# Kernel optimization log

Hardware: AMD Instinct MI355X
Metric: run time of the kernel (lower is better)

## Reference

```python
import jax, jax.numpy as jnp
import numpy as np

NU, NM, E, L, B = 20000, 10000, 64, 3, 8192
SLOPE = 0.01  # torch leaky_relu default negative_slope


def _xavier(key, shape):
    fan_in, fan_out = shape[-1], shape[-2] if len(shape) >= 2 else shape[-1]
    limit = np.sqrt(6.0 / (fan_in + fan_out)).astype(np.float32)
    return jax.random.uniform(key, shape, jnp.float32, -limit, limit)


def setup_inputs() -> dict:
    key = jax.random.key(0)
    ks = jax.random.split(key, 12)
    user_adj = jax.random.uniform(ks[0], (NU, NM), jnp.float32)
    movie_adj = jax.random.uniform(ks[1], (NM, NU), jnp.float32)
    user_id = jax.random.randint(ks[2], (B,), 0, NU)
    movie_id = jax.random.randint(ks[3], (B,), 0, NM)
    user_emb = _xavier(ks[4], (NU, E))
    movie_emb = _xavier(ks[5], (NM, E))
    user_Ws = _xavier(ks[6], (L, E, E))
    user_bs = jnp.zeros((L, E), jnp.float32)
    movie_Ws = _xavier(ks[7], (L, E, E))
    movie_bs = jnp.zeros((L, E), jnp.float32)
    out_W = _xavier(ks[8], ((L + 1) * E, 1))
    out_b = jnp.zeros((1,), jnp.float32)
    return {
        "user_adj": user_adj, "movie_adj": movie_adj,
        "user_id": user_id, "movie_id": movie_id,
        "user_emb": user_emb, "movie_emb": movie_emb,
        "user_Ws": user_Ws, "user_bs": user_bs,
        "movie_Ws": movie_Ws, "movie_bs": movie_bs,
        "out_W": out_W, "out_b": out_b,
    }


def reference(user_adj, movie_adj, user_id, movie_id,
              user_emb, movie_emb, user_Ws, user_bs,
              movie_Ws, movie_bs, out_W, out_b):
    # dropout=0, carry_alpha=0, use_agate=False -> layer-0 embeddings are the tables
    us = [user_emb]   # list of [NU, E]
    ms = [movie_emb]  # list of [NM, E]
    n_layers = user_Ws.shape[0]
    for l in range(n_layers):
        # layer(adj @ other) + layer(self) == (adj @ other + self) @ W.T + 2*b
        u_new = jax.nn.leaky_relu(
            (user_adj @ ms[-1] + us[-1]) @ user_Ws[l].T + 2.0 * user_bs[l], SLOPE)
        m_new = jax.nn.leaky_relu(
            (movie_adj @ us[-1] + ms[-1]) @ movie_Ws[l].T + 2.0 * movie_bs[l], SLOPE)
        us.append(u_new)
        ms.append(m_new)
    # gather per-interaction embeddings at every depth, multiply, concat -> [B,(L+1)*E]
    inter = jnp.concatenate([u[user_id] * m[movie_id] for u, m in zip(us, ms)], axis=1)
    scores = (inter @ out_W + out_b).reshape(-1)  # [B]
    return scores, us[-1], ms[-1]
```

## Files before the change

### kernel.cpp

```cpp
#include <hip/hip_runtime.h>
#include <hip/hip_bf16.h>

typedef __attribute__((ext_vector_type(4))) float f32x4;
typedef __attribute__((ext_vector_type(8))) short short8;
typedef __attribute__((ext_vector_type(8))) __bf16 bf16x8;
typedef __attribute__((ext_vector_type(8))) unsigned char u8x8;

union FragU { bf16x8 h; short8 s; };
union F8 { f32x4 v[2]; float f[8]; };

typedef const __attribute__((address_space(1))) void gvoid_t;
typedef __attribute__((address_space(3))) void lvoid_t;

static __device__ __forceinline__ void gload16(const void* g, void* l) {
  __builtin_amdgcn_global_load_lds((gvoid_t*)g, (lvoid_t*)l, 16, 0, 0);
}

static __device__ __forceinline__ short8 cvt8(const f32x4 a0, const f32x4 a1) {
  bf16x8 hv;
  hv[0] = (__bf16)a0[0]; hv[1] = (__bf16)a0[1];
  hv[2] = (__bf16)a0[2]; hv[3] = (__bf16)a0[3];
  hv[4] = (__bf16)a1[0]; hv[5] = (__bf16)a1[1];
  hv[6] = (__bf16)a1[2]; hv[7] = (__bf16)a1[3];
  FragU u; u.h = hv; return u.s;
}

static __device__ __forceinline__ unsigned long long pack8_u8(
    const f32x4 a0, const f32x4 a1) {
  F8 u; u.v[0] = a0; u.v[1] = a1;
  unsigned long long r = 0;
  #pragma unroll
  for (int j = 0; j < 8; ++j) {
    unsigned int q = (unsigned int)(u.f[j] * 255.f + 0.5f);
    r |= (unsigned long long)(q & 255u) << (8 * j);
  }
  return r;
}

__global__ __launch_bounds__(256) void gemm_l0(
    const float* __restrict__ Au, const __bf16* __restrict__ BTu,
    unsigned char* __restrict__ AcU, float* __restrict__ Pu,
    int Mu, int Ku, int KTu, int padKu,
    const float* __restrict__ Am, const __bf16* __restrict__ BTm,
    unsigned char* __restrict__ AcM, float* __restrict__ Pm,
    int Mm, int Km, int KTm, int padKm,
    int nbU, int rbU, int rbM)
{
  __shared__ float  sA[2][4096];
  __shared__ __bf16 sB[2][2048];

  const int t = threadIdx.x;
  const int w = t >> 6;
  const int lane = t & 63;
  const int r = lane & 15;
  const int g = lane >> 4;

  const float* A; const __bf16* BT; unsigned char* Ac; float* P;
  int M, K, KT, Kpad, rowBlk, split;
  {
    int bx = blockIdx.x;
    if (bx < nbU) {
      A = Au; BT = BTu; Ac = AcU; P = Pu; M = Mu; K = Ku; KT = KTu; Kpad = padKu;
      rowBlk = bx % rbU; split = bx / rbU;
    } else {
      int b2 = bx - nbU;
      A = Am; BT = BTm; Ac = AcM; P = Pm; M = Mm; K = Km; KT = KTm; Kpad = padKm;
      rowBlk = b2 % rbM; split = b2 / rbM;
    }
  }
  const int rowBase = rowBlk * 128;
  const int NS = Kpad >> 5;
  const int s0 = split * 64;
  const int ns = min(64, NS - s0);

  f32x4 acc[2][4];
  #pragma unroll
  for (int m = 0; m < 2; ++m)
    #pragma unroll
    for (int n = 0; n < 4; ++n)
      acc[m][n] = (f32x4){0.f, 0.f, 0.f, 0.f};

  const float* aRowP[4];
  int aOff[4];
  #pragma unroll
  for (int i = 0; i < 4; ++i) {
    int idx = i * 256 + t;
    int rr = idx >> 3;
    int p  = idx & 7;
    int rowg = rowBase + rr; if (rowg > M - 1) rowg = M - 1;
    aRowP[i] = A + (size_t)rowg * K;
    aOff[i] = (p ^ (rr & 7)) << 2;
  }
  const __bf16* bSrc = BT + (size_t)(w * 16 + (lane >> 2)) * Kpad
                     + (size_t)(((lane & 3) ^ ((lane >> 3) & 3)) * 8);

  auto stage = [&](int buf, int h) {
    const int kk = (s0 + h) * 32;
    #pragma unroll
    for (int i = 0; i < 4; ++i) {
      int ke = kk + aOff[i];
      if (ke > K - 4) ke = K - 4;
      gload16(aRowP[i] + ke, &sA[buf][i * 1024 + w * 256]);
    }
    gload16(bSrc + kk, &sB[buf][w * 512]);
  };

  auto cons = [&](int buf, int h) {
    const int k32 = s0 + h;
    const bool ok = (k32 * 32 + g * 8) < K;
    const short8 z8 = {0, 0, 0, 0, 0, 0, 0, 0};
    FragU aF[2], bF[4];
    unsigned long long a8[2];
    #pragma unroll
    for (int m = 0; m < 2; ++m) {
      const float* rowp = &sA[buf][(w * 32 + m * 16 + r) * 32];
      f32x4 a0 = *(const f32x4*)(rowp + (((2 * g)     ^ (r & 7)) << 2));
      f32x4 a1 = *(const f32x4*)(rowp + (((2 * g + 1) ^ (r & 7)) << 2));
      aF[m].s = ok ? cvt8(a0, a1) : z8;
      a8[m] = ok ? pack8_u8(a0, a1) : 0ull;
    }
    const int gb = g ^ ((r >> 1) & 3);
    #pragma unroll
    for (int n = 0; n < 4; ++n)
      bF[n].s = *(const short8*)&sB[buf][(n * 16 + r) * 32 + gb * 8];
    #pragma unroll
    for (int m = 0; m < 2; ++m)
      #pragma unroll
      for (int n = 0; n < 4; ++n)
        acc[m][n] = __builtin_amdgcn_mfma_f32_16x16x32_bf16(
            aF[m].s, bF[n].s, acc[m][n], 0, 0, 0);
    const int kt = k32 >> 1, ks = k32 & 1;
    unsigned char* cp = Ac + ((size_t)rowBlk * KT + kt) * 8192
                      + (size_t)ks * 4096 + (size_t)lane * 8;
    *(unsigned long long*)(cp + (w * 2 + 0) * 512) = a8[0];
    *(unsigned long long*)(cp + (w * 2 + 1) * 512) = a8[1];
  };

  stage(0, 0);

  for (int h = 0; h < ns; ++h) {
    asm volatile("s_waitcnt vmcnt(0)" ::: "memory");
    __builtin_amdgcn_s_barrier();
    asm volatile("" ::: "memory");
    if (h + 1 < ns) stage((h + 1) & 1, h + 1);
    cons(h & 1, h);
  }

  float* Pp = P + (size_t)split * M * 64;
  #pragma unroll
  for (int m = 0; m < 2; ++m) {
    #pragma unroll
    for (int j = 0; j < 4; ++j) {
      const int row = rowBase + w * 32 + m * 16 + g * 4 + j;
      if (row < M) {
        #pragma unroll
        for (int n = 0; n < 4; ++n)
          Pp[(size_t)row * 64 + n * 16 + r] = acc[m][n][j];
      }
    }
  }
}

__global__ __launch_bounds__(256) void gemm_l12(
    const unsigned char* __restrict__ AcU, const __bf16* __restrict__ BTu,
    float* __restrict__ Pu, int Mu, int KTu, int padKu,
    const unsigned char* __restrict__ AcM, const __bf16* __restrict__ BTm,
    float* __restrict__ Pm, int Mm, int KTm, int padKm,
    int nbU, int rbU, int rbM, int SPS)
{
  __shared__ unsigned char sA[2][8192];
  __shared__ __bf16 sB[2][4096];

  const int t = threadIdx.x;
  const int w = t >> 6;
  const int lane = t & 63;
  const int r = lane & 15;
  const int g = lane >> 4;

  const unsigned char* Ac; const __bf16* BT; float* P;
  int M, KT, Kpad, rowBlk, split;
  {
    int bx = blockIdx.x;
    if (bx < nbU) {
      Ac = AcU; BT = BTu; P = Pu; M = Mu; KT = KTu; Kpad = padKu;
      rowBlk = bx % rbU; split = bx / rbU;
    } else {
      int b2 = bx - nbU;
      Ac = AcM; BT = BTm; P = Pm; M = Mm; KT = KTm; Kpad = padKm;
      rowBlk = b2 % rbM; split = b2 / rbM;
    }
  }
  const int rowBase = rowBlk * 128;
  const int s0 = split * SPS;
  const int ns = min(SPS, KT - s0);

  f32x4 acc[2][4];
  #pragma unroll
  for (int m = 0; m < 2; ++m)
    #pragma unroll
    for (int n = 0; n < 4; ++n)
      acc[m][n] = (f32x4){0.f, 0.f, 0.f, 0.f};

  const unsigned char* aB = Ac + (size_t)rowBlk * KT * 8192
                          + (size_t)w * 1024 + (size_t)lane * 16;
  const int browl = w * 16 + (lane >> 2);
  const int bgr = (lane & 3) ^ ((browl >> 1) & 3);
  const __bf16* bB = BT + (size_t)browl * Kpad + (size_t)bgr * 8;

  auto stage = [&](int buf, int hh) {
    const size_t tb = (size_t)(s0 + hh) * 8192;
    gload16(aB + tb,        &sA[buf][w * 1024]);
    gload16(aB + tb + 4096, &sA[buf][4096 + w * 1024]);
    const int k0 = (s0 + hh) * 64;
    gload16(bB + k0,      &sB[buf][w * 512]);
    gload16(bB + k0 + 32, &sB[buf][2048 + w * 512]);
  };

  auto cons = [&](int buf) {
    FragU aF[2][2], bF[2][4];
    #pragma unroll
    for (int ks = 0; ks < 2; ++ks) {
      #pragma unroll
      for (int m = 0; m < 2; ++m) {
        u8x8 by = *(const u8x8*)&sA[buf][ks * 4096 + (w * 2 + m) * 512 + lane * 8];
        bf16x8 hv;
        #pragma unroll
        for (int j = 0; j < 8; ++j) hv[j] = (__bf16)(float)by[j];
        aF[ks][m].h = hv;
      }
      #pragma unroll
      for (int n = 0; n < 4; ++n) {
        const int rowl = n * 16 + r;
        const int gg = g ^ ((rowl >> 1) & 3);
        bF[ks][n].s = *(const short8*)&sB[buf][ks * 2048 + rowl * 32 + gg * 8];
      }
    }
    #pragma unroll
    for (int ks = 0; ks < 2; ++ks)
      #pragma unroll
      for (int m = 0; m < 2; ++m)
        #pragma unroll
        for (int n = 0; n < 4; ++n)
          acc[m][n] = __builtin_amdgcn_mfma_f32_16x16x32_bf16(
              aF[ks][m].s, bF[ks][n].s, acc[m][n], 0, 0, 0);
  };

  stage(0, 0);

  for (int h = 0; h < ns; ++h) {
    asm volatile("s_waitcnt vmcnt(0)" ::: "memory");
    __builtin_amdgcn_s_barrier();
    asm volatile("" ::: "memory");
    if (h + 1 < ns) stage((h + 1) & 1, h + 1);
    cons(h & 1);
  }

  const float inv = 1.f / 255.f;
  float* Pp = P + (size_t)split * M * 64;
  #pragma unroll
  for (int m = 0; m < 2; ++m) {
    #pragma unroll
    for (int j = 0; j < 4; ++j) {
      const int row = rowBase + w * 32 + m * 16 + g * 4 + j;
      if (row < M) {
        #pragma unroll
        for (int n = 0; n < 4; ++n)
          Pp[(size_t)row * 64 + n * 16 + r] = acc[m][n][j] * inv;
      }
    }
  }
}

__global__ __launch_bounds__(256) void transpose_cvt(
    const float* __restrict__ in, __bf16* __restrict__ out, int K, int Kpad)
{
  __shared__ float tile[64][65];
  const int t = threadIdx.x;
  const int k0 = blockIdx.x * 64;
  #pragma unroll
  for (int i = 0; i < 4; ++i) {
    int f = t + i * 256;
    int k = f >> 4;
    int cc = (f & 15) << 2;
    if (k0 + k < K) {
      f32x4 v = *(const f32x4*)(in + (size_t)(k0 + k) * 64 + cc);
      tile[k][cc + 0] = v[0]; tile[k][cc + 1] = v[1];
      tile[k][cc + 2] = v[2]; tile[k][cc + 3] = v[3];
    }
  }
  __syncthreads();
  const int c = t >> 2;
  const int kc = (t & 3) << 4;
  #pragma unroll
  for (int h = 0; h < 2; ++h) {
    int kk = kc + h * 8;
    FragU p;
    if (k0 + kk < K) {
      #pragma unroll
      for (int j = 0; j < 8; ++j) p.h[j] = (__bf16)tile[kk + j][c];
    } else {
      p.s = (short8){0,0,0,0,0,0,0,0};
    }
    *(short8*)(out + (size_t)c * Kpad + k0 + kk) = p.s;
  }
}

__global__ __launch_bounds__(256) void layer_reduce(
    const float* __restrict__ P, int S,
    const float* __restrict__ self, const float* __restrict__ W,
    const float* __restrict__ b, float* __restrict__ out, int M)
{
  __shared__ float xs[4][64];
  const int t = threadIdx.x;
  const int c = t & 63;
  const int grp = t >> 6;
  const int row = blockIdx.x * 4 + grp;
  if (row < M) {
    float x = self[(size_t)row * 64 + c];
    for (int s = 0; s < S; ++s)
      x += P[(size_t)s * M * 64 + (size_t)row * 64 + c];
    xs[grp][c] = x;
  }
  __syncthreads();
  if (row >= M) return;
  float acc = 0.f;
  const f32x4* Wc = (const f32x4*)(W + c * 64);
  #pragma unroll
  for (int k4 = 0; k4 < 16; ++k4) {
    f32x4 wv = Wc[k4];
    acc += xs[grp][k4 * 4 + 0] * wv[0] + xs[grp][k4 * 4 + 1] * wv[1]
         + xs[grp][k4 * 4 + 2] * wv[2] + xs[grp][k4 * 4 + 3] * wv[3];
  }
  float v = acc + 2.0f * b[c];
  out[(size_t)row * 64 + c] = (v > 0.f) ? v : 0.01f * v;
}

__global__ __launch_bounds__(256) void gather_score(
    const int* __restrict__ uid, const int* __restrict__ mid,
    const float* __restrict__ u0, const float* __restrict__ u1,
    const float* __restrict__ u2, const float* __restrict__ u3,
    const float* __restrict__ m0, const float* __restrict__ m1,
    const float* __restrict__ m2, const float* __restrict__ m3,
    const float* __restrict__ oW, const float* __restrict__ ob,
    float* __restrict__ scores, int B)
{
  const int wave = threadIdx.x >> 6;
  const int lane = threadIdx.x & 63;
  const int b = blockIdx.x * 4 + wave;
  if (b >= B) return;
  const size_t ub = (size_t)uid[b] * 64 + lane;
  const size_t mb = (size_t)mid[b] * 64 + lane;
  float acc = u0[ub] * m0[mb] * oW[lane]
            + u1[ub] * m1[mb] * oW[64 + lane]
            + u2[ub] * m2[mb] * oW[128 + lane]
            + u3[ub] * m3[mb] * oW[192 + lane];
  #pragma unroll
  for (int off = 32; off > 0; off >>= 1)
    acc += __shfl_down(acc, off, 64);
  if (lane == 0) scores[b] = acc + ob[0];
}

extern "C" void kernel_launch(void* const* d_in, const int* in_sizes, int n_in,
                              void* d_out, int out_size, void* d_ws, size_t ws_size,
                              hipStream_t stream)
{
  const float* user_adj  = (const float*)d_in[0];
  const float* movie_adj = (const float*)d_in[1];
  const int*   user_id   = (const int*)d_in[2];
  const int*   movie_id  = (const int*)d_in[3];
  const float* user_emb  = (const float*)d_in[4];
  const float* movie_emb = (const float*)d_in[5];
  const float* user_Ws   = (const float*)d_in[6];
  const float* user_bs   = (const float*)d_in[7];
  const float* movie_Ws  = (const float*)d_in[8];
  const float* movie_bs  = (const float*)d_in[9];
  const float* out_W     = (const float*)d_in[10];
  const float* out_b     = (const float*)d_in[11];

  const int NU = 20000, NM = 10000, E = 64, B = 8192;
  const int rbU = 157, rbM = 79;
  const int KT_U = 157, KT_M = 313;
  const int NMpad = KT_U * 64;
  const int NUpad = KT_M * 64;
  const int SU = 5, SM = 10;
  const int SPS12 = 32;

  char* ws = (char*)d_ws;
  size_t o = 0;
  unsigned char* Au8 = (unsigned char*)(ws + o); o += (size_t)rbU * KT_U * 8192;
  unsigned char* Am8 = (unsigned char*)(ws + o); o += (size_t)rbM * KT_M * 8192;
  float*  uP  = (float*)(ws + o);  o += (size_t)SU * NU * 64 * 4;
  float*  mP  = (float*)(ws + o);  o += (size_t)SM * NM * 64 * 4;
  float*  u1  = (float*)(ws + o);  o += (size_t)NU * 64 * 4;
  float*  u2  = (float*)(ws + o);  o += (size_t)NU * 64 * 4;
  float*  m1  = (float*)(ws + o);  o += (size_t)NM * 64 * 4;
  float*  m2  = (float*)(ws + o);  o += (size_t)NM * 64 * 4;
  __bf16* uT  = (__bf16*)(ws + o); o += (size_t)64 * NUpad * 2;
  __bf16* mT  = (__bf16*)(ws + o); o += (size_t)64 * NMpad * 2;

  float* scores = (float*)d_out;
  float* u3 = scores + B;
  float* m3 = u3 + (size_t)NU * E;

  const int nbU = rbU * SU;
  const int nbM = rbM * SM;

  const float* uCur = user_emb;
  const float* mCur = movie_emb;
  for (int l = 0; l < 3; ++l) {
    float* uNext = (l == 0) ? u1 : (l == 1) ? u2 : u3;
    float* mNext = (l == 0) ? m1 : (l == 1) ? m2 : m3;

    transpose_cvt<<<NMpad / 64, 256, 0, stream>>>(mCur, mT, NM, NMpad);
    transpose_cvt<<<NUpad / 64, 256, 0, stream>>>(uCur, uT, NU, NUpad);

    if (l == 0) {
      gemm_l0<<<nbU + nbM, 256, 0, stream>>>(
          user_adj, mT, Au8, uP, NU, NM, KT_U, NMpad,
          movie_adj, uT, Am8, mP, NM, NU, KT_M, NUpad,
          nbU, rbU, rbM);
    } else {
      gemm_l12<<<nbU + nbM, 256, 0, stream>>>(
          Au8, mT, uP, NU, KT_U, NMpad,
          Am8, uT, mP, NM, KT_M, NUpad,
          nbU, rbU, rbM, SPS12);
    }

    layer_reduce<<<(NU + 3) / 4, 256, 0, stream>>>(
        uP, SU, uCur, user_Ws + (size_t)l * E * E, user_bs + (size_t)l * E, uNext, NU);
    layer_reduce<<<(NM + 3) / 4, 256, 0, stream>>>(
        mP, SM, mCur, movie_Ws + (size_t)l * E * E, movie_bs + (size_t)l * E, mNext, NM);
    uCur = uNext; mCur = mNext;
  }
  gather_score<<<(B + 3) / 4, 256, 0, stream>>>(
      user_id, movie_id, user_emb, u1, u2, u3,
      movie_emb, m1, m2, m3, out_W, out_b, scores, B);
}
```

Baseline: 907.6 us.

## Swizzle blocks across XCDs, retune split-K, fuse transpose into layer_reduce

Adds an XCD-aware block index swizzle to both GEMM kernels so blocks placed on the same XCD share locality. Retunes the split-K partitioning: fewer, longer splits for layer 0, and separate split sizes for the user and movie sides in layers 1-2. Removes the transpose_cvt launches for layers 1-2 by having layer_reduce write the bf16 transposed copy of its output directly, which saves a read pass but produces strided, uncoalesced 2-byte stores.

Result: slower. 929.8 us (+2.4%).

```diff
diff --git a/kernel.cpp b/kernel.cpp
--- a/kernel.cpp
+++ b/kernel.cpp
@@ -37,6 +37,12 @@
   return r;
 }
 
+static __device__ __forceinline__ int xcd_swz(int orig, int nwg) {
+  const int xcd = orig & 7, loc = orig >> 3;
+  const int q = nwg >> 3, rr = nwg & 7;
+  return (xcd < rr ? xcd * (q + 1) : rr * (q + 1) + (xcd - rr) * q) + loc;
+}
+
 __global__ __launch_bounds__(256) void gemm_l0(
     const float* __restrict__ Au, const __bf16* __restrict__ BTu,
     unsigned char* __restrict__ AcU, float* __restrict__ Pu,
@@ -44,7 +50,7 @@
     const float* __restrict__ Am, const __bf16* __restrict__ BTm,
     unsigned char* __restrict__ AcM, float* __restrict__ Pm,
     int Mm, int Km, int KTm, int padKm,
-    int nbU, int rbU, int rbM)
+    int nbU, int rbU, int rbM, int SPS)
 {
   __shared__ float  sA[2][4096];
   __shared__ __bf16 sB[2][2048];
@@ -58,7 +64,7 @@
   const float* A; const __bf16* BT; unsigned char* Ac; float* P;
   int M, K, KT, Kpad, rowBlk, split;
   {
-    int bx = blockIdx.x;
+    int bx = xcd_swz(blockIdx.x, gridDim.x);
     if (bx < nbU) {
       A = Au; BT = BTu; Ac = AcU; P = Pu; M = Mu; K = Ku; KT = KTu; Kpad = padKu;
       rowBlk = bx % rbU; split = bx / rbU;
@@ -70,8 +76,8 @@
   }
   const int rowBase = rowBlk * 128;
   const int NS = Kpad >> 5;
-  const int s0 = split * 64;
-  const int ns = min(64, NS - s0);
+  const int s0 = split * SPS;
+  const int ns = min(SPS, NS - s0);
 
   f32x4 acc[2][4];
   #pragma unroll
@@ -166,7 +172,7 @@
     float* __restrict__ Pu, int Mu, int KTu, int padKu,
     const unsigned char* __restrict__ AcM, const __bf16* __restrict__ BTm,
     float* __restrict__ Pm, int Mm, int KTm, int padKm,
-    int nbU, int rbU, int rbM, int SPS)
+    int nbU, int rbU, int rbM, int SPSu, int SPSm)
 {
   __shared__ unsigned char sA[2][8192];
   __shared__ __bf16 sB[2][4096];
@@ -178,16 +184,16 @@
   const int g = lane >> 4;
 
   const unsigned char* Ac; const __bf16* BT; float* P;
-  int M, KT, Kpad, rowBlk, split;
+  int M, KT, Kpad, rowBlk, split, SPS;
   {
-    int bx = blockIdx.x;
+    int bx = xcd_swz(blockIdx.x, gridDim.x);
     if (bx < nbU) {
       Ac = AcU; BT = BTu; P = Pu; M = Mu; KT = KTu; Kpad = padKu;
-      rowBlk = bx % rbU; split = bx / rbU;
+      rowBlk = bx % rbU; split = bx / rbU; SPS = SPSu;
     } else {
       int b2 = bx - nbU;
       Ac = AcM; BT = BTm; P = Pm; M = Mm; KT = KTm; Kpad = padKm;
-      rowBlk = b2 % rbM; split = b2 / rbM;
+      rowBlk = b2 % rbM; split = b2 / rbM; SPS = SPSm;
     }
   }
   const int rowBase = rowBlk * 128;
@@ -308,7 +314,8 @@
 __global__ __launch_bounds__(256) void layer_reduce(
     const float* __restrict__ P, int S,
     const float* __restrict__ self, const float* __restrict__ W,
-    const float* __restrict__ b, float* __restrict__ out, int M)
+    const float* __restrict__ b, float* __restrict__ out,
+    __bf16* __restrict__ outT, int Kpad, int M)
 {
   __shared__ float xs[4][64];
   const int t = threadIdx.x;
@@ -332,7 +339,9 @@
          + xs[grp][k4 * 4 + 2] * wv[2] + xs[grp][k4 * 4 + 3] * wv[3];
   }
   float v = acc + 2.0f * b[c];
-  out[(size_t)row * 64 + c] = (v > 0.f) ? v : 0.01f * v;
+  v = (v > 0.f) ? v : 0.01f * v;
+  out[(size_t)row * 64 + c] = v;
+  if (Kpad > 0) outT[(size_t)c * Kpad + row] = (__bf16)v;
 }
 
 __global__ __launch_bounds__(256) void gather_score(
@@ -382,15 +391,16 @@
   const int KT_U = 157, KT_M = 313;
   const int NMpad = KT_U * 64;
   const int NUpad = KT_M * 64;
-  const int SU = 5, SM = 10;
-  const int SPS12 = 32;
+  const int SU0 = 3, SM0 = 6, SPS0 = 105;
+  const int SU1 = 5, SM1 = 9;
+  const int SPS1u = 32, SPS1m = 35;
 
   char* ws = (char*)d_ws;
   size_t o = 0;
   unsigned char* Au8 = (unsigned char*)(ws + o); o += (size_t)rbU * KT_U * 8192;
   unsigned char* Am8 = (unsigned char*)(ws + o); o += (size_t)rbM * KT_M * 8192;
-  float*  uP  = (float*)(ws + o);  o += (size_t)SU * NU * 64 * 4;
-  float*  mP  = (float*)(ws + o);  o += (size_t)SM * NM * 64 * 4;
+  float*  uP  = (float*)(ws + o);  o += (size_t)SU1 * NU * 64 * 4;
+  float*  mP  = (float*)(ws + o);  o += (size_t)SM1 * NM * 64 * 4;
   float*  u1  = (float*)(ws + o);  o += (size_t)NU * 64 * 4;
   float*  u2  = (float*)(ws + o);  o += (size_t)NU * 64 * 4;
   float*  m1  = (float*)(ws + o);  o += (size_t)NM * 64 * 4;
@@ -402,34 +412,42 @@
   float* u3 = scores + B;
   float* m3 = u3 + (size_t)NU * E;
 
-  const int nbU = rbU * SU;
-  const int nbM = rbM * SM;
-
-  const float* uCur = user_emb;
-  const float* mCur = movie_emb;
-  for (int l = 0; l < 3; ++l) {
-    float* uNext = (l == 0) ? u1 : (l == 1) ? u2 : u3;
-    float* mNext = (l == 0) ? m1 : (l == 1) ? m2 : m3;
-
-    transpose_cvt<<<NMpad / 64, 256, 0, stream>>>(mCur, mT, NM, NMpad);
-    transpose_cvt<<<NUpad / 64, 256, 0, stream>>>(uCur, uT, NU, NUpad);
-
-    if (l == 0) {
-      gemm_l0<<<nbU + nbM, 256, 0, stream>>>(
-          user_adj, mT, Au8, uP, NU, NM, KT_U, NMpad,
-          movie_adj, uT, Am8, mP, NM, NU, KT_M, NUpad,
-          nbU, rbU, rbM);
-    } else {
-      gemm_l12<<<nbU + nbM, 256, 0, stream>>>(
-          Au8, mT, uP, NU, KT_U, NMpad,
-          Am8, uT, mP, NM, KT_M, NUpad,
-          nbU, rbU, rbM, SPS12);
-    }
+  const int nbU0 = rbU * SU0;
+  const int nbM0 = rbM * SM0;
+  const int nbU1 = rbU * SU1;
+  const int nbM1 = rbM * SM1;
+
+  transpose_cvt<<<NMpad / 64, 256, 0, stream>>>(movie_emb, mT, NM, NMpad);
+  transpose_cvt<<<NUpad / 64, 256, 0, stream>>>(user_emb, uT, NU, NUpad);
+
+  gemm_l0<<<nbU0 + nbM0, 256, 0, stream>>>(
+      user_adj, mT, Au8, uP, NU, NM, KT_U, NMpad,
+      movie_adj, uT, Am8, mP, NM, NU, KT_M, NUpad,
+      nbU0, rbU, rbM, SPS0);
+
+  layer_reduce<<<(NU + 3) / 4, 256, 0, stream>>>(
+      uP, SU0, user_emb, user_Ws, user_bs, u1, uT, NUpad, NU);
+  layer_reduce<<<(NM + 3) / 4, 256, 0, stream>>>(
+      mP, SM0, movie_emb, movie_Ws, movie_bs, m1, mT, NMpad, NM);
+
+  const float* uCur = u1;
+  const float* mCur = m1;
+  for (int l = 1; l < 3; ++l) {
+    float* uNext = (l == 1) ? u2 : u3;
+    float* mNext = (l == 1) ? m2 : m3;
+    const int wT = (l == 1) ? 1 : 0;
+
+    gemm_l12<<<nbU1 + nbM1, 256, 0, stream>>>(
+        Au8, mT, uP, NU, KT_U, NMpad,
+        Am8, uT, mP, NM, KT_M, NUpad,
+        nbU1, rbU, rbM, SPS1u, SPS1m);
 
     layer_reduce<<<(NU + 3) / 4, 256, 0, stream>>>(
-        uP, SU, uCur, user_Ws + (size_t)l * E * E, user_bs + (size_t)l * E, uNext, NU);
+        uP, SU1, uCur, user_Ws + (size_t)l * E * E, user_bs + (size_t)l * E,
+        uNext, uT, wT ? NUpad : 0, NU);
     layer_reduce<<<(NM + 3) / 4, 256, 0, stream>>>(
-        mP, SM, mCur, movie_Ws + (size_t)l * E * E, movie_bs + (size_t)l * E, mNext, NM);
+        mP, SM1, mCur, movie_Ws + (size_t)l * E * E, movie_bs + (size_t)l * E,
+        mNext, mT, wT ? NMpad : 0, NM);
     uCur = uNext; mCur = mNext;
   }
   gather_score<<<(B + 3) / 4, 256, 0, stream>>>(
```
